# Optimization experiments

Measured on AMD Instinct MI355X. Metric: run time of the kernel, lower is better.

Reference implementation:

```python
import jax, jax.numpy as jnp
import numpy as np


def _hadamard(n: int) -> np.ndarray:
    # Sylvester construction; n must be a power of 2 (asserted in the torch source).
    H = np.array([[1.0]], dtype=np.float32)
    while H.shape[0] < n:
        H = np.block([[H, H], [H, -H]])
    return (H * (n ** -0.5)).astype(np.float32)


def _rotate_activation(x):
    # hadamard_transform(x, scale=D**-0.5) over the last dim; bf16 in/out like the CUDA kernel.
    D = x.shape[-1]
    H = jnp.asarray(_hadamard(D))
    return (x.astype(jnp.float32) @ H).astype(x.dtype)


def _cu_seqlen_kv_bounds(seq_lens, num_ctx_tokens):
    # Vectorized equivalent of compute_cu_seqlen_kv_bounds_nocache (repeat_interleave -> searchsorted).
    offsets = jnp.concatenate([jnp.zeros(1, jnp.int32), jnp.cumsum(seq_lens).astype(jnp.int32)])
    pos = jnp.arange(num_ctx_tokens, dtype=jnp.int32)
    batch_ids = jnp.searchsorted(offsets, pos, side='right').astype(jnp.int32) - 1
    ks = offsets[batch_ids]                 # start of this token's sequence in packed KV
    ke = ks + (pos - ks) + 1                # causal: local_position + 1 past the start
    return ks, ke


def setup_inputs() -> dict:
    key = jax.random.key(0)
    k1, k2, k3 = jax.random.split(key, 3)
    T, H, D = 2048, 16, 128
    q = jax.random.normal(k1, (T, H, D), dtype=jnp.bfloat16)
    k = jax.random.normal(k2, (T, D), dtype=jnp.bfloat16)
    weights = jax.random.uniform(k3, (T, H), dtype=jnp.float32) * (H ** -0.5)
    seq_lens = jnp.array([1024, 1024], dtype=jnp.int32)
    return {"q": q, "k": k, "weights": weights, "seq_lens": seq_lens, "index_topk": 256}


def reference(q, k, weights, seq_lens, index_topk):
    T = q.shape[0]
    # Hadamard-rotate q and k (lightning indexer activation rotation).
    qr = _rotate_activation(q).astype(jnp.float32)   # [T, H, D]
    kr = _rotate_activation(k).astype(jnp.float32)   # [T, D]
    # Index score: I[t, s] = sum_h w[t, h] * relu(q[t, h] . k[s])
    logits = jnp.einsum('thd,sd->ths', qr, kr)       # [T, H, T]
    scores = jnp.einsum('ths,th->ts', jax.nn.relu(logits), weights)  # [T, T]
    # Causal ragged-batch KV window per token.
    ks, ke = _cu_seqlen_kv_bounds(seq_lens, T)
    pos = jnp.arange(T, dtype=jnp.int32)
    valid = (pos[None, :] >= ks[:, None]) & (pos[None, :] < ke[:, None])
    NEG = jnp.float32(-1e30)
    masked = jnp.where(valid, scores, NEG)
    topk_vals, topk_idx = jax.lax.top_k(masked, index_topk)  # [T, topk]
    return topk_vals, topk_idx
```

## Files before the change

### kernel.cpp

```cpp
#include <hip/hip_runtime.h>
#include <hip/hip_bf16.h>
#include <stdint.h>

typedef __attribute__((ext_vector_type(8))) short short8;
typedef __attribute__((ext_vector_type(4))) float float4_t;
typedef __attribute__((ext_vector_type(16))) float float16_t;

#define DDIM 128
#define SORTN 256
#define LROW 136
#define SCAP 1088
#define NCHT 17

__device__ inline unsigned short f32_to_bf16_rne(float f) {
    uint32_t u = __float_as_uint(f);
    return (unsigned short)((u + 0x7FFFu + ((u >> 16) & 1u)) >> 16);
}
__device__ inline float bf16_to_f32(unsigned short h) {
    return __uint_as_float(((uint32_t)h) << 16);
}
__device__ inline int ks_of(const int* seq_lens, int n_seq, int t) {
    int off = 0, r = 0;
    for (int i = 0; i < n_seq; ++i) {
        int nx = off + seq_lens[i];
        if (t < nx) { r = off; break; }
        off = nx;
    }
    return r;
}

__device__ inline int wave_reduce_add_dpp(int x) {
    x += __builtin_amdgcn_update_dpp(0, x, 0x111, 0xF, 0xF, true);
    x += __builtin_amdgcn_update_dpp(0, x, 0x112, 0xF, 0xF, true);
    x += __builtin_amdgcn_update_dpp(0, x, 0x114, 0xF, 0xF, true);
    x += __builtin_amdgcn_update_dpp(0, x, 0x118, 0xF, 0xF, true);
    x += __builtin_amdgcn_update_dpp(0, x, 0x142, 0xA, 0xF, true);
    x += __builtin_amdgcn_update_dpp(0, x, 0x143, 0xC, 0xF, true);
    return __builtin_amdgcn_readlane(x, 63);
}

__global__ __launch_bounds__(256) void rotate_k_kernel(
        const unsigned short* __restrict__ k, unsigned short* __restrict__ kr, int T) {
    int row = blockIdx.x * 16 + (threadIdx.x >> 4);
    if (row >= T) return;
    int l16 = threadIdx.x & 15;
    short8 in = *(const short8*)(k + (size_t)row * DDIM + 8 * l16);
    float f[8];
    #pragma unroll
    for (int j = 0; j < 8; ++j) f[j] = bf16_to_f32((unsigned short)in[j]);
    #pragma unroll
    for (int b = 1; b <= 4; b <<= 1)
        #pragma unroll
        for (int j = 0; j < 8; ++j)
            if (!(j & b)) { float a = f[j], c = f[j | b]; f[j] = a + c; f[j | b] = a - c; }
    #pragma unroll
    for (int m = 1; m <= 8; m <<= 1) {
        bool hi = (l16 & m) != 0;
        #pragma unroll
        for (int j = 0; j < 8; ++j) {
            float o = __shfl_xor(f[j], m, 64);
            f[j] = hi ? (o - f[j]) : (f[j] + o);
        }
    }
    const float sc = 0.08838834764831845f;
    short8 out;
    #pragma unroll
    for (int j = 0; j < 8; ++j) out[j] = (short)f32_to_bf16_rne(f[j] * sc);
    *(short8*)(kr + (size_t)row * DDIM + 8 * l16) = out;
}

__global__ __launch_bounds__(256, 2) void fused_kernel(
        const unsigned short* __restrict__ q,
        const unsigned short* __restrict__ kr,
        const float* __restrict__ w,
        const int* __restrict__ seq_lens, int n_seq,
        float* __restrict__ out_vals, float* __restrict__ out_idx,
        int T, int H, int K, int Tt) {
    __shared__ __align__(16) unsigned short bL[2][64 * LROW];
    __shared__ __align__(16) float scw[4][SCAP];
    unsigned short* qst = (unsigned short*)&scw[0][0];

    const int tid  = threadIdx.x;
    const int wv   = tid >> 6, lane = tid & 63;
    const int pair = wv & 1, rowtile = wv >> 1;
    const int col  = lane & 15, kgrp = lane >> 4;
    const int hi   = lane >> 5;
    const int srow = tid >> 4, sseg = tid & 15;

    const int m     = blockIdx.x;
    const int ttile = (m & 1) ? (Tt - 1 - (m >> 1)) : (m >> 1);
    const int tt0   = ttile * 4;

    const int tAg = tt0 + pair * 2, tBg = tAg + 1;
    const bool vA = (tAg < T), vB = (tBg < T);
    const int tA  = vA ? tAg : T - 1, tB = vB ? tBg : T - 1;
    const int ksA = ks_of(seq_lens, n_seq, tA);
    const int ksB = ks_of(seq_lens, n_seq, tB);

    const int bks    = ks_of(seq_lens, n_seq, tt0);
    const int bke    = (tt0 + 4 < T) ? (tt0 + 4) : T;
    const int nchunk = (bke - bks + 63) >> 6;

    short8 pre[4];
    #pragma unroll
    for (int it = 0; it < 4; ++it) {
        int gs = bks + srow + 16 * it; if (gs > T - 1) gs = T - 1;
        pre[it] = *(const short8*)(kr + (size_t)gs * DDIM + sseg * 8);
    }

    const int t_r = (tt0 + wv < T) ? (tt0 + wv) : (T - 1);
    float f[4][8];
    const unsigned short* qrow = q + ((size_t)t_r * H + col) * DDIM + kgrp * 8;
    #pragma unroll
    for (int kk = 0; kk < 4; ++kk) {
        short8 v = *(const short8*)(qrow + kk * 32);
        #pragma unroll
        for (int j = 0; j < 8; ++j) f[kk][j] = bf16_to_f32((unsigned short)v[j]);
    }
    #pragma unroll
    for (int b = 1; b <= 4; b <<= 1)
        #pragma unroll
        for (int kk = 0; kk < 4; ++kk)
            #pragma unroll
            for (int j = 0; j < 8; ++j)
                if (!(j & b)) { float a = f[kk][j], c = f[kk][j | b];
                                f[kk][j] = a + c; f[kk][j | b] = a - c; }
    #pragma unroll
    for (int kk = 0; kk < 4; ++kk)
        #pragma unroll
        for (int j = 0; j < 8; ++j) {
            float o = __shfl_xor(f[kk][j], 16, 64);
            f[kk][j] = (kgrp & 1) ? (o - f[kk][j]) : (f[kk][j] + o);
        }
    #pragma unroll
    for (int kk = 0; kk < 4; ++kk)
        #pragma unroll
        for (int j = 0; j < 8; ++j) {
            float o = __shfl_xor(f[kk][j], 32, 64);
            f[kk][j] = (kgrp & 2) ? (o - f[kk][j]) : (f[kk][j] + o);
        }
    #pragma unroll
    for (int j = 0; j < 8; ++j) {
        { float a = f[0][j], c = f[1][j]; f[0][j] = a + c; f[1][j] = a - c; }
        { float a = f[2][j], c = f[3][j]; f[2][j] = a + c; f[3][j] = a - c; }
        { float a = f[0][j], c = f[2][j]; f[0][j] = a + c; f[2][j] = a - c; }
        { float a = f[1][j], c = f[3][j]; f[1][j] = a + c; f[3][j] = a - c; }
    }
    const float scl = 0.08838834764831845f;
    #pragma unroll
    for (int kk = 0; kk < 4; ++kk) {
        short8 o;
        #pragma unroll
        for (int j = 0; j < 8; ++j) o[j] = (short)f32_to_bf16_rne(f[kk][j] * scl);
        *(short8*)&qst[(wv * 16 + col) * LROW + kgrp * 8 + kk * 32] = o;
    }

    #pragma unroll
    for (int it = 0; it < 4; ++it)
        *(short8*)&bL[0][(srow + 16 * it) * LROW + sseg * 8] = pre[it];
    __syncthreads();

    short8 afrag[8];
    {
        const unsigned short* qr2 = qst + (pair * 32 + (lane & 31)) * LROW + hi * 8;
        #pragma unroll
        for (int k8 = 0; k8 < 8; ++k8) afrag[k8] = *(const short8*)(qr2 + 16 * k8);
    }
    float wAr[8], wBr[8];
    #pragma unroll
    for (int r = 0; r < 8; ++r) {
        int h = (r & 3) + 8 * ((r >> 2) & 1) + 4 * hi;
        wAr[r] = w[(size_t)tA * H + h];
        wBr[r] = w[(size_t)tB * H + h];
    }
    __syncthreads();

    const int nrow = rowtile * 32 + (lane & 31);
    for (int c = 0; c < nchunk; ++c) {
        const int kv0 = bks + c * 64;
        if (c + 1 < nchunk) {
            int kvn = kv0 + 64;
            #pragma unroll
            for (int it = 0; it < 4; ++it) {
                int gs = kvn + srow + 16 * it; if (gs > T - 1) gs = T - 1;
                pre[it] = *(const short8*)(kr + (size_t)gs * DDIM + sseg * 8);
            }
        }
        const unsigned short* brow = &bL[c & 1][nrow * LROW + hi * 8];
        float16_t acc = {0.f, 0.f, 0.f, 0.f, 0.f, 0.f, 0.f, 0.f,
                         0.f, 0.f, 0.f, 0.f, 0.f, 0.f, 0.f, 0.f};
        __builtin_amdgcn_s_setprio(1);
        #pragma unroll
        for (int k8 = 0; k8 < 8; ++k8) {
            short8 bf = *(const short8*)(brow + 16 * k8);
            acc = __builtin_amdgcn_mfma_f32_32x32x16_bf16(afrag[k8], bf, acc, 0, 0, 0);
        }
        __builtin_amdgcn_s_setprio(0);
        float pA = 0.f, pB = 0.f;
        #pragma unroll
        for (int r = 0; r < 8; ++r) {
            float va = acc[r];     va = va > 0.f ? va : 0.f; pA += wAr[r] * va;
            float vb = acc[r + 8]; vb = vb > 0.f ? vb : 0.f; pB += wBr[r] * vb;
        }
        pA += __shfl_xor(pA, 32, 64);
        pB += __shfl_xor(pB, 32, 64);
        const int s = kv0 + nrow;
        if (hi == 0) {
            if (vA && s >= ksA && s <= tA) scw[pair * 2][s - ksA] = pA;
        } else {
            if (vB && s >= ksB && s <= tB) scw[pair * 2 + 1][s - ksB] = pB;
        }
        if (c + 1 < nchunk) {
            #pragma unroll
            for (int it = 0; it < 4; ++it)
                *(short8*)&bL[(c + 1) & 1][(srow + 16 * it) * LROW + sseg * 8] = pre[it];
        }
        __syncthreads();
    }

    const int t_s = tt0 + wv;
    if (t_s >= T) return;
    const int ks_w = ks_of(seq_lens, n_seq, t_s);
    const int ke_w = t_s + 1;
    const int n    = ke_w - ks_w;

    const int nch = (n + 63) >> 6;
    uint32_t ukey[NCHT];
    #pragma unroll
    for (int c = 0; c < NCHT; ++c) {
        if (c < nch) {
            int i = c * 64 + lane;
            ukey[c] = (i < n) ? __float_as_uint(scw[wv][i]) : 0u;
        } else ukey[c] = 0u;
    }
    unsigned long long* candw = (unsigned long long*)&scw[wv][0];

    const int Keff = (n < K) ? n : K;
    uint32_t ustar = 0;
    int ttake = K;
    if (n > K) {
        uint32_t lo = 0, hia = 0x80000000u;
        for (int it = 0; it < 31; ++it) {
            uint32_t mid = (lo + hia) >> 1;
            int lc = 0;
            #pragma unroll
            for (int c = 0; c < NCHT; ++c)
                if (c < nch) lc += (ukey[c] >= mid) ? 1 : 0;
            int total = wave_reduce_add_dpp(lc);
            if (total >= K) lo = mid; else hia = mid;
        }
        ustar = lo;
        int lg = 0;
        #pragma unroll
        for (int c = 0; c < NCHT; ++c)
            if (c < nch) lg += (ukey[c] > ustar) ? 1 : 0;
        ttake = K - wave_reduce_add_dpp(lg);
    }

    {
        const unsigned long long ltm = (1ull << lane) - 1ull;
        int base = 0, tieBase = 0;
        const bool selAll = (n <= K);
        #pragma unroll
        for (int c = 0; c < NCHT; ++c) {
            if (c < nch) {
                int i = c * 64 + lane;
                bool inb = (i < n);
                uint32_t u = ukey[c];
                bool isGt  = inb && (selAll || u > ustar);
                bool isTie = inb && !selAll && (u == ustar);
                unsigned long long mt = __ballot(isTie);
                int tr = tieBase + (int)__popcll(mt & ltm);
                bool take = isGt || (isTie && tr < ttake);
                unsigned long long mk = __ballot(take);
                if (take) {
                    int pos = base + (int)__popcll(mk & ltm);
                    int s = ks_w + i;
                    if (pos < SORTN)
                        candw[pos] = ((((unsigned long long)u << 11) |
                                       (unsigned long long)(T - 1 - s)) + 1ull);
                }
                base    += (int)__popcll(mk);
                tieBase += (int)__popcll(mt);
            }
        }
        for (int i = Keff + lane; i < SORTN; i += 64) candw[i] = 0ull;
    }

    unsigned long long kreg[4];
    #pragma unroll
    for (int r = 0; r < 4; ++r) kreg[r] = candw[4 * lane + r];

    #define CX(a, b, dsc) { unsigned long long _mx = (a) > (b) ? (a) : (b); \
                            unsigned long long _mn = (a) > (b) ? (b) : (a); \
                            (a) = (dsc) ? _mx : _mn; (b) = (dsc) ? _mn : _mx; }
    #pragma unroll
    for (int size = 2; size <= SORTN; size <<= 1) {
        #pragma unroll
        for (int stride = SORTN >> 1; stride >= 4; stride >>= 1) {
            if (stride > (size >> 1)) continue;
            int lmask = stride >> 2;
            #pragma unroll
            for (int r = 0; r < 4; ++r) {
                int e = 4 * lane + r;
                unsigned long long other = __shfl_xor(kreg[r], lmask, 64);
                bool desc = ((e & size) == 0);
                bool iAmLow = ((e & stride) == 0);
                bool keepMax = (iAmLow == desc);
                kreg[r] = keepMax ? (kreg[r] > other ? kreg[r] : other)
                                  : (kreg[r] < other ? kreg[r] : other);
            }
        }
        if (size >= 4) {
            bool d = (((4 * lane) & size) == 0);
            CX(kreg[0], kreg[2], d);
            CX(kreg[1], kreg[3], d);
            CX(kreg[0], kreg[1], d);
            CX(kreg[2], kreg[3], d);
        } else {
            CX(kreg[0], kreg[1], true);
            CX(kreg[2], kreg[3], false);
        }
    }
    #undef CX

    if (4 * lane < K) {
        float4_t v4, i4;
        #pragma unroll
        for (int r = 0; r < 4; ++r) {
            int e = 4 * lane + r;
            unsigned long long key = kreg[r];
            float v; int idx;
            if (key != 0ull) {
                unsigned long long km1 = key - 1ull;
                v = __uint_as_float((uint32_t)(km1 >> 11));
                idx = T - 1 - (int)(km1 & 0x7FFull);
            } else {
                int pidx = e - Keff;
                idx = (pidx < ks_w) ? pidx : (ke_w + (pidx - ks_w));
                v = -1e30f;
            }
            v4[r] = v; i4[r] = (float)idx;
        }
        *(float4_t*)(out_vals + (size_t)t_s * K + 4 * lane) = v4;
        *(float4_t*)(out_idx  + (size_t)t_s * K + 4 * lane) = i4;
    }
}

extern "C" void kernel_launch(void* const* d_in, const int* in_sizes, int n_in,
                              void* d_out, int out_size, void* d_ws, size_t ws_size,
                              hipStream_t stream) {
    const unsigned short* q = (const unsigned short*)d_in[0];
    const unsigned short* k = (const unsigned short*)d_in[1];
    const float* w          = (const float*)d_in[2];
    const int* seq_lens     = (const int*)d_in[3];
    const int n_seq = in_sizes[3];
    const int T = in_sizes[1] / DDIM;
    const int H = in_sizes[2] / T;
    const int K = out_size / (2 * T);

    unsigned short* kr = (unsigned short*)d_ws;
    float* out_vals = (float*)d_out;
    float* out_idx  = out_vals + (size_t)T * K;

    rotate_k_kernel<<<dim3((T + 15) / 16), dim3(256), 0, stream>>>(k, kr, T);
    const int Tt = (T + 3) / 4;
    fused_kernel<<<dim3(Tt), dim3(256), 0, stream>>>(
        q, kr, w, seq_lens, n_seq, out_vals, out_idx, T, H, K, Tt);
}
```

Before: 101.2 us.

## Process 128-row KV chunks per wave with both query pairs sharing B fragments

Each wave now covers 32 KV rows of a 128-row chunk and runs two MFMAs per k-step, one per query pair, against the same B fragment. The old split had each pair of waves handle 64 rows for a single query pair. This halves the number of chunk iterations and barriers and reuses each LDS B load for both pairs. LDS double buffering is replaced by a single buffer that is written at the top of each iteration, followed by an extra barrier. The block-to-tile mapping also changes from interleaved to split halves, and register pressure rises from the extra A fragments, accumulators and weights.

After: 99.73 us, median of 2. Within noise of the previous version (-1.5%).

```diff
diff --git a/kernel.cpp b/kernel.cpp
--- a/kernel.cpp
+++ b/kernel.cpp
@@ -76,36 +76,40 @@
         const int* __restrict__ seq_lens, int n_seq,
         float* __restrict__ out_vals, float* __restrict__ out_idx,
         int T, int H, int K, int Tt) {
-    __shared__ __align__(16) unsigned short bL[2][64 * LROW];
+    __shared__ __align__(16) unsigned short bL[128 * LROW];
     __shared__ __align__(16) float scw[4][SCAP];
     unsigned short* qst = (unsigned short*)&scw[0][0];
 
     const int tid  = threadIdx.x;
     const int wv   = tid >> 6, lane = tid & 63;
-    const int pair = wv & 1, rowtile = wv >> 1;
     const int col  = lane & 15, kgrp = lane >> 4;
     const int hi   = lane >> 5;
+    const int l31  = lane & 31;
     const int srow = tid >> 4, sseg = tid & 15;
 
     const int m     = blockIdx.x;
-    const int ttile = (m & 1) ? (Tt - 1 - (m >> 1)) : (m >> 1);
+    const int halfG = Tt >> 1;
+    const int ttile = (Tt <= 1) ? 0 : ((m < halfG) ? m : (Tt - 1 - (m - halfG)));
     const int tt0   = ttile * 4;
 
-    const int tAg = tt0 + pair * 2, tBg = tAg + 1;
-    const bool vA = (tAg < T), vB = (tBg < T);
-    const int tA  = vA ? tAg : T - 1, tB = vB ? tBg : T - 1;
-    const int ksA = ks_of(seq_lens, n_seq, tA);
-    const int ksB = ks_of(seq_lens, n_seq, tB);
+    const int tg1 = tt0 + 1, tg2 = tt0 + 2, tg3 = tt0 + 3;
+    const bool v0 = (tt0 < T), v1 = (tg1 < T), v2 = (tg2 < T), v3 = (tg3 < T);
+    const int t0 = v0 ? tt0 : T - 1, t1 = v1 ? tg1 : T - 1;
+    const int t2 = v2 ? tg2 : T - 1, t3 = v3 ? tg3 : T - 1;
+    const int ks0 = ks_of(seq_lens, n_seq, t0);
+    const int ks1 = ks_of(seq_lens, n_seq, t1);
+    const int ks2 = ks_of(seq_lens, n_seq, t2);
+    const int ks3 = ks_of(seq_lens, n_seq, t3);
 
     const int bks    = ks_of(seq_lens, n_seq, tt0);
     const int bke    = (tt0 + 4 < T) ? (tt0 + 4) : T;
-    const int nchunk = (bke - bks + 63) >> 6;
-
-    short8 pre[4];
-    #pragma unroll
-    for (int it = 0; it < 4; ++it) {
-        int gs = bks + srow + 16 * it; if (gs > T - 1) gs = T - 1;
-        pre[it] = *(const short8*)(kr + (size_t)gs * DDIM + sseg * 8);
+    const int nchunk = (bke - bks + 127) >> 7;
+
+    short8 pre[8];
+    #pragma unroll
+    for (int i = 0; i < 8; ++i) {
+        int gs = bks + srow + 16 * i; if (gs > T - 1) gs = T - 1;
+        pre[i] = *(const short8*)(kr + (size_t)gs * DDIM + sseg * 8);
     }
 
     const int t_r = (tt0 + wv < T) ? (tt0 + wv) : (T - 1);
@@ -154,66 +158,76 @@
         for (int j = 0; j < 8; ++j) o[j] = (short)f32_to_bf16_rne(f[kk][j] * scl);
         *(short8*)&qst[(wv * 16 + col) * LROW + kgrp * 8 + kk * 32] = o;
     }
-
-    #pragma unroll
-    for (int it = 0; it < 4; ++it)
-        *(short8*)&bL[0][(srow + 16 * it) * LROW + sseg * 8] = pre[it];
     __syncthreads();
 
-    short8 afrag[8];
+    short8 afrag0[8], afrag1[8];
     {
-        const unsigned short* qr2 = qst + (pair * 32 + (lane & 31)) * LROW + hi * 8;
-        #pragma unroll
-        for (int k8 = 0; k8 < 8; ++k8) afrag[k8] = *(const short8*)(qr2 + 16 * k8);
-    }
-    float wAr[8], wBr[8];
+        const unsigned short* qr0 = qst + l31 * LROW + hi * 8;
+        const unsigned short* qr1 = qst + (32 + l31) * LROW + hi * 8;
+        #pragma unroll
+        for (int k8 = 0; k8 < 8; ++k8) {
+            afrag0[k8] = *(const short8*)(qr0 + 16 * k8);
+            afrag1[k8] = *(const short8*)(qr1 + 16 * k8);
+        }
+    }
+    float w0r[8], w1r[8], w2r[8], w3r[8];
     #pragma unroll
     for (int r = 0; r < 8; ++r) {
         int h = (r & 3) + 8 * ((r >> 2) & 1) + 4 * hi;
-        wAr[r] = w[(size_t)tA * H + h];
-        wBr[r] = w[(size_t)tB * H + h];
+        w0r[r] = w[(size_t)t0 * H + h];
+        w1r[r] = w[(size_t)t1 * H + h];
+        w2r[r] = w[(size_t)t2 * H + h];
+        w3r[r] = w[(size_t)t3 * H + h];
     }
     __syncthreads();
 
-    const int nrow = rowtile * 32 + (lane & 31);
+    const int nrow = wv * 32 + l31;
     for (int c = 0; c < nchunk; ++c) {
-        const int kv0 = bks + c * 64;
+        const int kv0 = bks + (c << 7);
+        #pragma unroll
+        for (int i = 0; i < 8; ++i)
+            *(short8*)&bL[(srow + 16 * i) * LROW + sseg * 8] = pre[i];
+        __syncthreads();
         if (c + 1 < nchunk) {
-            int kvn = kv0 + 64;
+            int kvn = kv0 + 128;
             #pragma unroll
-            for (int it = 0; it < 4; ++it) {
-                int gs = kvn + srow + 16 * it; if (gs > T - 1) gs = T - 1;
-                pre[it] = *(const short8*)(kr + (size_t)gs * DDIM + sseg * 8);
+            for (int i = 0; i < 8; ++i) {
+                int gs = kvn + srow + 16 * i; if (gs > T - 1) gs = T - 1;
+                pre[i] = *(const short8*)(kr + (size_t)gs * DDIM + sseg * 8);
             }
         }
-        const unsigned short* brow = &bL[c & 1][nrow * LROW + hi * 8];
-        float16_t acc = {0.f, 0.f, 0.f, 0.f, 0.f, 0.f, 0.f, 0.f,
-                         0.f, 0.f, 0.f, 0.f, 0.f, 0.f, 0.f, 0.f};
+        const unsigned short* brow = &bL[nrow * LROW + hi * 8];
+        float16_t acc01 = {0.f, 0.f, 0.f, 0.f, 0.f, 0.f, 0.f, 0.f,
+                           0.f, 0.f, 0.f, 0.f, 0.f, 0.f, 0.f, 0.f};
+        float16_t acc23 = {0.f, 0.f, 0.f, 0.f, 0.f, 0.f, 0.f, 0.f,
+                           0.f, 0.f, 0.f, 0.f, 0.f, 0.f, 0.f, 0.f};
         __builtin_amdgcn_s_setprio(1);
         #pragma unroll
         for (int k8 = 0; k8 < 8; ++k8) {
             short8 bf = *(const short8*)(brow + 16 * k8);
-            acc = __builtin_amdgcn_mfma_f32_32x32x16_bf16(afrag[k8], bf, acc, 0, 0, 0);
+            acc01 = __builtin_amdgcn_mfma_f32_32x32x16_bf16(afrag0[k8], bf, acc01, 0, 0, 0);
+            acc23 = __builtin_amdgcn_mfma_f32_32x32x16_bf16(afrag1[k8], bf, acc23, 0, 0, 0);
         }
         __builtin_amdgcn_s_setprio(0);
-        float pA = 0.f, pB = 0.f;
+        float p0 = 0.f, p1 = 0.f, p2 = 0.f, p3 = 0.f;
         #pragma unroll
         for (int r = 0; r < 8; ++r) {
-            float va = acc[r];     va = va > 0.f ? va : 0.f; pA += wAr[r] * va;
-            float vb = acc[r + 8]; vb = vb > 0.f ? vb : 0.f; pB += wBr[r] * vb;
-        }
-        pA += __shfl_xor(pA, 32, 64);
-        pB += __shfl_xor(pB, 32, 64);
+            float a = acc01[r];     a = a > 0.f ? a : 0.f; p0 += w0r[r] * a;
+            float b = acc01[r + 8]; b = b > 0.f ? b : 0.f; p1 += w1r[r] * b;
+            float g = acc23[r];     g = g > 0.f ? g : 0.f; p2 += w2r[r] * g;
+            float d = acc23[r + 8]; d = d > 0.f ? d : 0.f; p3 += w3r[r] * d;
+        }
+        p0 += __shfl_xor(p0, 32, 64);
+        p1 += __shfl_xor(p1, 32, 64);
+        p2 += __shfl_xor(p2, 32, 64);
+        p3 += __shfl_xor(p3, 32, 64);
         const int s = kv0 + nrow;
         if (hi == 0) {
-            if (vA && s >= ksA && s <= tA) scw[pair * 2][s - ksA] = pA;
+            if (v0 && s >= ks0 && s <= t0) scw[0][s - ks0] = p0;
+            if (v2 && s >= ks2 && s <= t2) scw[2][s - ks2] = p2;
         } else {
-            if (vB && s >= ksB && s <= tB) scw[pair * 2 + 1][s - ksB] = pB;
-        }
-        if (c + 1 < nchunk) {
-            #pragma unroll
-            for (int it = 0; it < 4; ++it)
-                *(short8*)&bL[(c + 1) & 1][(srow + 16 * it) * LROW + sseg * 8] = pre[it];
+            if (v1 && s >= ks1 && s <= t1) scw[1][s - ks1] = p1;
+            if (v3 && s >= ks3 && s <= t3) scw[3][s - ks3] = p3;
         }
         __syncthreads();
     }
```
